# Optimization experiments

Measured on AMD Instinct MI355X. Metric: run time of the kernel, lower is better.

Reference implementation:

```python
import jax, jax.numpy as jnp
import numpy as np

N_NODES = 100000
N_EDGES = 6400000
D_IN = 512
D_HID = 16
N_CLASSES = 16


def setup_inputs() -> dict:
    key = jax.random.key(0)
    k1, k2, k3, k4, k5, k6 = jax.random.split(key, 6)
    x = jax.random.normal(k1, (N_NODES, D_IN), dtype=jnp.float32)
    edge_index = jax.random.randint(k2, (2, N_EDGES), 0, N_NODES, dtype=jnp.int64)
    # Glorot-style init for GCN weights
    W1 = jax.random.normal(k3, (D_IN, D_HID), dtype=jnp.float32) * (1.0 / np.sqrt(D_IN))
    b1 = jnp.zeros((D_HID,), dtype=jnp.float32)
    W2 = jax.random.normal(k4, (D_HID, N_CLASSES), dtype=jnp.float32) * (1.0 / np.sqrt(D_HID))
    b2 = jnp.zeros((N_CLASSES,), dtype=jnp.float32)
    return {"x": x, "W1": W1, "b1": b1, "W2": W2, "b2": b2, "edge_index": edge_index}


def reference(x, W1, b1, W2, b2, edge_index):
    N = x.shape[0]
    loops = jnp.arange(N, dtype=edge_index.dtype)
    # GCN: add self-loops, symmetric D^-1/2 A D^-1/2 normalization
    src = jnp.concatenate([edge_index[0], loops])  # [E+N]
    dst = jnp.concatenate([edge_index[1], loops])  # [E+N]
    deg = jax.ops.segment_sum(jnp.ones(src.shape[0], dtype=x.dtype), dst, num_segments=N)
    dinv = jnp.where(deg > 0, jax.lax.rsqrt(deg), 0.0)
    norm = (dinv[src] * dinv[dst])[:, None]  # [E+N, 1]

    def gcn_conv(h, W, b):
        h = h @ W                                  # [N, d_out] transform first (PyG order)
        agg = jax.ops.segment_sum(h[src] * norm, dst, num_segments=N)
        return agg + b

    h = jax.nn.relu(gcn_conv(x, W1, b1))
    # F.dropout(training=self.training) is identity in eval mode
    logits = gcn_conv(h, W2, b2)
    return jax.nn.log_softmax(logits, axis=1)
```

## Files before the change

kernel.cpp:

```cpp
#include <hip/hip_runtime.h>
#include <hip/hip_bf16.h>
#include <math.h>

#define N_NODES 100000
#define N_EDGES 6400000
#define D_IN 512
#define D_HID 16

__global__ void deg_kernel(const int* __restrict__ dst, int* __restrict__ deg) {
    int e = blockIdx.x * blockDim.x + threadIdx.x;
    if (e < N_EDGES) atomicAdd(&deg[dst[e]], 1);
}

__global__ void dinv_kernel(const int* __restrict__ deg, float* __restrict__ dinv) {
    int i = blockIdx.x * blockDim.x + threadIdx.x;
    if (i < N_NODES) dinv[i] = rsqrtf((float)deg[i] + 1.0f);
}

__global__ void scan1(const int* __restrict__ deg, int* __restrict__ row_start,
                      int* __restrict__ bsum) {
    __shared__ int sd[256];
    int tid = threadIdx.x;
    int base = blockIdx.x * 1024 + tid * 4;
    int d0 = 0, d1 = 0, d2 = 0, d3 = 0;
    if (base + 3 < N_NODES) {
        d0 = deg[base]; d1 = deg[base + 1]; d2 = deg[base + 2]; d3 = deg[base + 3];
    } else {
        if (base < N_NODES) d0 = deg[base];
        if (base + 1 < N_NODES) d1 = deg[base + 1];
        if (base + 2 < N_NODES) d2 = deg[base + 2];
    }
    int s = d0 + d1 + d2 + d3;
    sd[tid] = s;
    __syncthreads();
    for (int off = 1; off < 256; off <<= 1) {
        int v = (tid >= off) ? sd[tid - off] : 0;
        __syncthreads();
        sd[tid] += v;
        __syncthreads();
    }
    int excl = sd[tid] - s;
    if (base < N_NODES) row_start[base] = excl;
    if (base + 1 < N_NODES) row_start[base + 1] = excl + d0;
    if (base + 2 < N_NODES) row_start[base + 2] = excl + d0 + d1;
    if (base + 3 < N_NODES) row_start[base + 3] = excl + d0 + d1 + d2;
    if (tid == 255) bsum[blockIdx.x] = sd[255];
}

__global__ void scan2(int* __restrict__ bsum, int nb) {
    __shared__ int sd[128];
    int tid = threadIdx.x;
    int v = (tid < nb) ? bsum[tid] : 0;
    sd[tid] = v;
    __syncthreads();
    for (int off = 1; off < 128; off <<= 1) {
        int u = (tid >= off) ? sd[tid - off] : 0;
        __syncthreads();
        sd[tid] += u;
        __syncthreads();
    }
    if (tid < nb) bsum[tid] = sd[tid] - v;
}

__global__ void scan3(int* __restrict__ row_start, int* __restrict__ cursor,
                      const int* __restrict__ bsum) {
    int off = bsum[blockIdx.x];
    int base = blockIdx.x * 1024 + threadIdx.x * 4;
#pragma unroll
    for (int j = 0; j < 4; j++) {
        int i = base + j;
        if (i < N_NODES) {
            int v = row_start[i] + off;
            row_start[i] = v;
            cursor[i] = v;
        }
    }
}

__global__ void fill_csr(const int* __restrict__ src, const int* __restrict__ dst,
                         int* __restrict__ cursor, int* __restrict__ csr) {
    int e = blockIdx.x * blockDim.x + threadIdx.x;
    if (e < N_EDGES) {
        int d = dst[e];
        int pos = atomicAdd(&cursor[d], 1);
        csr[pos] = src[e];
    }
}

__global__ __launch_bounds__(256) void gemm1(const float* __restrict__ x,
                                             const float* __restrict__ W1,
                                             float* __restrict__ h1) {
    __shared__ float xs[256 * 33];
    int tid = threadIdx.x;
    int row0 = blockIdx.x * 256;
    int row = row0 + tid;
    float acc[16];
#pragma unroll
    for (int c = 0; c < 16; c++) acc[c] = 0.f;

    for (int k0 = 0; k0 < D_IN; k0 += 32) {
        __syncthreads();
#pragma unroll
        for (int l = 0; l < 8; l++) {
            int idx = tid + l * 256;
            int r = idx >> 3;
            int f4 = idx & 7;
            int gr = row0 + r;
            float4 v = make_float4(0.f, 0.f, 0.f, 0.f);
            if (gr < N_NODES)
                v = *(const float4*)(x + (size_t)gr * D_IN + k0 + f4 * 4);
            int a = r * 33 + f4 * 4;
            xs[a] = v.x; xs[a + 1] = v.y; xs[a + 2] = v.z; xs[a + 3] = v.w;
        }
        __syncthreads();
#pragma unroll
        for (int kk = 0; kk < 32; kk++) {
            float xv = xs[tid * 33 + kk];
            const float* wr = W1 + (k0 + kk) * 16;
#pragma unroll
            for (int c = 0; c < 16; c++) acc[c] = fmaf(xv, wr[c], acc[c]);
        }
    }
    if (row < N_NODES) {
        float4* o = (float4*)(h1 + (size_t)row * 16);
        o[0] = make_float4(acc[0], acc[1], acc[2], acc[3]);
        o[1] = make_float4(acc[4], acc[5], acc[6], acc[7]);
        o[2] = make_float4(acc[8], acc[9], acc[10], acc[11]);
        o[3] = make_float4(acc[12], acc[13], acc[14], acc[15]);
    }
}

__global__ __launch_bounds__(256) void agg1(const float* __restrict__ h1,
                                            const float* __restrict__ dinv,
                                            const int* __restrict__ row_start,
                                            const int* __restrict__ deg,
                                            const int* __restrict__ csr,
                                            const float* __restrict__ b1,
                                            const float* __restrict__ W2,
                                            float* __restrict__ h3) {
    int tid = threadIdx.x;
    int node = blockIdx.x * 16 + (tid >> 4);
    int c = tid & 15;
    if (node >= N_NODES) return;
    float di = dinv[node];
    float acc = h1[(size_t)node * 16 + c] * di * di;
    int start = row_start[node];
    int cnt = deg[node];
    int sN = 0; float vN = 0.f, dN = 0.f;
    if (cnt > 0) {
        sN = csr[start];
        vN = h1[(size_t)sN * 16 + c];
        dN = dinv[sN];
    }
    for (int t = 0; t < cnt; t++) {
        float vC = vN, dC = dN;
        if (t + 1 < cnt) {
            int s = csr[start + t + 1];
            vN = h1[(size_t)s * 16 + c];
            dN = dinv[s];
        }
        acc = fmaf(vC, dC * di, acc);
    }
    float v = acc + b1[c];
    v = v > 0.f ? v : 0.f;
    float out = 0.f;
#pragma unroll
    for (int j = 0; j < 16; j++) {
        float vj = __shfl(v, j, 16);
        out = fmaf(vj, W2[j * 16 + c], out);
    }
    h3[(size_t)node * 16 + c] = out;
}

__global__ __launch_bounds__(256) void agg2(const float* __restrict__ h3,
                                            const float* __restrict__ dinv,
                                            const int* __restrict__ row_start,
                                            const int* __restrict__ deg,
                                            const int* __restrict__ csr,
                                            const float* __restrict__ b2,
                                            float* __restrict__ out) {
    int tid = threadIdx.x;
    int node = blockIdx.x * 16 + (tid >> 4);
    int c = tid & 15;
    if (node >= N_NODES) return;
    float di = dinv[node];
    float acc = h3[(size_t)node * 16 + c] * di * di;
    int start = row_start[node];
    int cnt = deg[node];
    int sN = 0; float vN = 0.f, dN = 0.f;
    if (cnt > 0) {
        sN = csr[start];
        vN = h3[(size_t)sN * 16 + c];
        dN = dinv[sN];
    }
    for (int t = 0; t < cnt; t++) {
        float vC = vN, dC = dN;
        if (t + 1 < cnt) {
            int s = csr[start + t + 1];
            vN = h3[(size_t)s * 16 + c];
            dN = dinv[s];
        }
        acc = fmaf(vC, dC * di, acc);
    }
    float logit = acc + b2[c];
    float m = logit;
#pragma unroll
    for (int mask = 1; mask < 16; mask <<= 1)
        m = fmaxf(m, __shfl_xor(m, mask, 16));
    float e = expf(logit - m);
    float ssum = e;
#pragma unroll
    for (int mask = 1; mask < 16; mask <<= 1)
        ssum += __shfl_xor(ssum, mask, 16);
    out[(size_t)node * 16 + c] = (logit - m) - logf(ssum);
}

extern "C" void kernel_launch(void* const* d_in, const int* in_sizes, int n_in,
                              void* d_out, int out_size, void* d_ws, size_t ws_size,
                              hipStream_t stream) {
    const float* x  = (const float*)d_in[0];
    const float* W1 = (const float*)d_in[1];
    const float* b1 = (const float*)d_in[2];
    const float* W2 = (const float*)d_in[3];
    const float* b2 = (const float*)d_in[4];
    const int*   ei = (const int*)d_in[5];
    const int* src = ei;
    const int* dst = ei + N_EDGES;
    float* out = (float*)d_out;

    int* deg       = (int*)d_ws;
    int* row_start = deg + 100096;
    int* cursor    = row_start + 100096;
    float* dinv    = (float*)(cursor + 100096);
    int* bsum      = (int*)(dinv + 100096);
    int* csr       = bsum + 128;
    float* h1      = (float*)(csr + N_EDGES);
    float* h3      = h1 + 1600000;

    hipMemsetAsync(deg, 0, N_NODES * sizeof(int), stream);
    deg_kernel<<<N_EDGES / 256, 256, 0, stream>>>(dst, deg);
    dinv_kernel<<<(N_NODES + 255) / 256, 256, 0, stream>>>(deg, dinv);
    scan1<<<98, 256, 0, stream>>>(deg, row_start, bsum);
    scan2<<<1, 128, 0, stream>>>(bsum, 98);
    scan3<<<98, 256, 0, stream>>>(row_start, cursor, bsum);
    fill_csr<<<N_EDGES / 256, 256, 0, stream>>>(src, dst, cursor, csr);
    gemm1<<<(N_NODES + 255) / 256, 256, 0, stream>>>(x, W1, h1);
    agg1<<<(N_NODES + 15) / 16, 256, 0, stream>>>(h1, dinv, row_start, deg, csr, b1, W2, h3);
    agg2<<<(N_NODES + 15) / 16, 256, 0, stream>>>(h3, dinv, row_start, deg, csr, b2, out);
}
```

Before: 1.519 ms.

## Build CSR via two-level bucketed counting sort with shared-memory atomics

Replaces the global per-node atomic degree count and atomic CSR fill with a two-pass bucket sort. Edges are first histogrammed into 391 buckets of 256 destination nodes using shared-memory atomics, then scattered into a packed (src<<8 | dst&255) buffer. Per-bucket blocks then compute degrees and place edges with shared-memory atomics. This aims to cut contended global random atomics and scattered writes, at the cost of an extra 25.6MB intermediate buffer plus extra passes over the edges. The packing assumes source ids fit in 24 bits.

```diff
diff --git a/kernel.cpp b/kernel.cpp
--- a/kernel.cpp
+++ b/kernel.cpp
@@ -6,10 +6,76 @@
 #define N_EDGES 6400000
 #define D_IN 512
 #define D_HID 16
-
-__global__ void deg_kernel(const int* __restrict__ dst, int* __restrict__ deg) {
-    int e = blockIdx.x * blockDim.x + threadIdx.x;
-    if (e < N_EDGES) atomicAdd(&deg[dst[e]], 1);
+#define NB 391
+
+__global__ __launch_bounds__(256) void khist(const int* __restrict__ dst,
+                                             int* __restrict__ bhist) {
+    __shared__ int h[NB];
+    int tid = threadIdx.x;
+    for (int i = tid; i < NB; i += 256) h[i] = 0;
+    __syncthreads();
+    int base = blockIdx.x * 25600;
+#pragma unroll 4
+    for (int k = 0; k < 100; k++) {
+        int e = base + k * 256 + tid;
+        atomicAdd(&h[dst[e] >> 8], 1);
+    }
+    __syncthreads();
+    for (int i = tid; i < NB; i += 256) atomicAdd(&bhist[i], h[i]);
+}
+
+__global__ void bscan(const int* __restrict__ bhist, int* __restrict__ bbase,
+                      int* __restrict__ bcur) {
+    __shared__ int sd[512];
+    int tid = threadIdx.x;
+    int v = (tid < NB) ? bhist[tid] : 0;
+    sd[tid] = v;
+    __syncthreads();
+    for (int off = 1; off < 512; off <<= 1) {
+        int u = (tid >= off) ? sd[tid - off] : 0;
+        __syncthreads();
+        sd[tid] += u;
+        __syncthreads();
+    }
+    if (tid < NB) {
+        int excl = sd[tid] - v;
+        bbase[tid] = excl;
+        bcur[tid] = excl;
+    }
+}
+
+__global__ __launch_bounds__(256) void kscatter(const int* __restrict__ src,
+                                                const int* __restrict__ dst,
+                                                int* __restrict__ bcur,
+                                                unsigned int* __restrict__ ebuf) {
+    int e = blockIdx.x * 256 + threadIdx.x;
+    int d = dst[e];
+    int s = src[e];
+    int b = d >> 8;
+    int pos = atomicAdd(&bcur[b], 1);
+    ebuf[pos] = ((unsigned int)s << 8) | (unsigned int)(d & 255);
+}
+
+__global__ __launch_bounds__(1024) void kdeg(const unsigned int* __restrict__ ebuf,
+                                             const int* __restrict__ bhist,
+                                             const int* __restrict__ bbase,
+                                             int* __restrict__ deg) {
+    __shared__ int h[256];
+    int tid = threadIdx.x;
+    int b = blockIdx.x;
+    if (tid < 256) h[tid] = 0;
+    __syncthreads();
+    int cnt = bhist[b];
+    int start = bbase[b];
+    for (int i = tid; i < cnt; i += 1024) {
+        unsigned int v = ebuf[start + i];
+        atomicAdd(&h[v & 255u], 1);
+    }
+    __syncthreads();
+    if (tid < 256) {
+        int node = b * 256 + tid;
+        if (node < N_NODES) deg[node] = h[tid];
+    }
 }
 
 __global__ void dinv_kernel(const int* __restrict__ deg, float* __restrict__ dinv) {
@@ -62,28 +128,35 @@
     if (tid < nb) bsum[tid] = sd[tid] - v;
 }
 
-__global__ void scan3(int* __restrict__ row_start, int* __restrict__ cursor,
-                      const int* __restrict__ bsum) {
+__global__ void scan3(int* __restrict__ row_start, const int* __restrict__ bsum) {
     int off = bsum[blockIdx.x];
     int base = blockIdx.x * 1024 + threadIdx.x * 4;
 #pragma unroll
     for (int j = 0; j < 4; j++) {
         int i = base + j;
-        if (i < N_NODES) {
-            int v = row_start[i] + off;
-            row_start[i] = v;
-            cursor[i] = v;
-        }
-    }
-}
-
-__global__ void fill_csr(const int* __restrict__ src, const int* __restrict__ dst,
-                         int* __restrict__ cursor, int* __restrict__ csr) {
-    int e = blockIdx.x * blockDim.x + threadIdx.x;
-    if (e < N_EDGES) {
-        int d = dst[e];
-        int pos = atomicAdd(&cursor[d], 1);
-        csr[pos] = src[e];
+        if (i < N_NODES) row_start[i] += off;
+    }
+}
+
+__global__ __launch_bounds__(1024) void kplace(const unsigned int* __restrict__ ebuf,
+                                               const int* __restrict__ bhist,
+                                               const int* __restrict__ bbase,
+                                               const int* __restrict__ row_start,
+                                               int* __restrict__ csr) {
+    __shared__ int cur[256];
+    int tid = threadIdx.x;
+    int b = blockIdx.x;
+    if (tid < 256) {
+        int node = b * 256 + tid;
+        cur[tid] = (node < N_NODES) ? row_start[node] : 0;
+    }
+    __syncthreads();
+    int cnt = bhist[b];
+    int start = bbase[b];
+    for (int i = tid; i < cnt; i += 1024) {
+        unsigned int v = ebuf[start + i];
+        int p = atomicAdd(&cur[v & 255u], 1);
+        csr[p] = (int)(v >> 8);
     }
 }
 
@@ -229,21 +302,27 @@
     float* out = (float*)d_out;
 
     int* deg       = (int*)d_ws;
-    int* row_start = deg + 100096;
-    int* cursor    = row_start + 100096;
-    float* dinv    = (float*)(cursor + 100096);
-    int* bsum      = (int*)(dinv + 100096);
-    int* csr       = bsum + 128;
+    int* row_start = deg + 100352;
+    float* dinv    = (float*)(row_start + 100352);
+    int* bsum      = (int*)(dinv + 100352);
+    int* bhist     = bsum + 128;
+    int* bbase     = bhist + 512;
+    int* bcur      = bbase + 512;
+    unsigned int* ebuf = (unsigned int*)(bcur + 512);
+    int* csr       = (int*)(ebuf + N_EDGES);
     float* h1      = (float*)(csr + N_EDGES);
     float* h3      = h1 + 1600000;
 
-    hipMemsetAsync(deg, 0, N_NODES * sizeof(int), stream);
-    deg_kernel<<<N_EDGES / 256, 256, 0, stream>>>(dst, deg);
+    hipMemsetAsync(bhist, 0, NB * sizeof(int), stream);
+    khist<<<250, 256, 0, stream>>>(dst, bhist);
+    bscan<<<1, 512, 0, stream>>>(bhist, bbase, bcur);
+    kscatter<<<N_EDGES / 256, 256, 0, stream>>>(src, dst, bcur, ebuf);
+    kdeg<<<NB, 1024, 0, stream>>>(ebuf, bhist, bbase, deg);
     dinv_kernel<<<(N_NODES + 255) / 256, 256, 0, stream>>>(deg, dinv);
     scan1<<<98, 256, 0, stream>>>(deg, row_start, bsum);
     scan2<<<1, 128, 0, stream>>>(bsum, 98);
-    scan3<<<98, 256, 0, stream>>>(row_start, cursor, bsum);
-    fill_csr<<<N_EDGES / 256, 256, 0, stream>>>(src, dst, cursor, csr);
+    scan3<<<98, 256, 0, stream>>>(row_start, bsum);
+    kplace<<<NB, 1024, 0, stream>>>(ebuf, bhist, bbase, row_start, csr);
     gemm1<<<(N_NODES + 255) / 256, 256, 0, stream>>>(x, W1, h1);
     agg1<<<(N_NODES + 15) / 16, 256, 0, stream>>>(h1, dinv, row_start, deg, csr, b1, W2, h3);
     agg2<<<(N_NODES + 15) / 16, 256, 0, stream>>>(h3, dinv, row_start, deg, csr, b2, out);
```

Result: slower. 3.046 ms (+100.5%).

## Replace per-node CSR build with bucketed edge partition and shared-memory atomic aggregation

Applied to the files above, without the earlier changes.

Edges are no longer sorted into a per-node CSR with global atomics. Instead, a block-local histogram and two-level scan scatter them into 128-node destination buckets, packing the source index and local destination into one word. Each aggregation block then accumulates its bucket's edges with LDS atomics, and rows are prescaled by dinv in the GEMM so the per-edge dinv gather is removed. This is meant to cut global atomic contention and the scattered CSR writes, at the cost of LDS atomic contention, a larger histogram workspace, and non-deterministic summation order.

```diff
diff --git a/kernel.cpp b/kernel.cpp
--- a/kernel.cpp
+++ b/kernel.cpp
@@ -7,89 +7,129 @@
 #define D_IN 512
 #define D_HID 16
 
-__global__ void deg_kernel(const int* __restrict__ dst, int* __restrict__ deg) {
-    int e = blockIdx.x * blockDim.x + threadIdx.x;
-    if (e < N_EDGES) atomicAdd(&deg[dst[e]], 1);
-}
-
-__global__ void dinv_kernel(const int* __restrict__ deg, float* __restrict__ dinv) {
-    int i = blockIdx.x * blockDim.x + threadIdx.x;
-    if (i < N_NODES) dinv[i] = rsqrtf((float)deg[i] + 1.0f);
-}
-
-__global__ void scan1(const int* __restrict__ deg, int* __restrict__ row_start,
-                      int* __restrict__ bsum) {
+#define NBKT 782
+#define NBP  784
+#define NBLK 1000
+#define EPB  6400
+
+__global__ __launch_bounds__(256) void khist(const int* __restrict__ dst,
+                                             int* __restrict__ hist_mat) {
+    __shared__ int h[NBP];
+    int tid = threadIdx.x;
+    int blk = blockIdx.x;
+    for (int i = tid; i < NBP; i += 256) h[i] = 0;
+    __syncthreads();
+    int base = blk * EPB;
+#pragma unroll
+    for (int k = 0; k < 25; k++)
+        atomicAdd(&h[dst[base + k * 256 + tid] >> 7], 1);
+    __syncthreads();
+    for (int i = tid; i < NBKT; i += 256) hist_mat[blk * NBP + i] = h[i];
+}
+
+__global__ __launch_bounds__(256) void kbtot(const int* __restrict__ hist_mat,
+                                             int* __restrict__ btot) {
     __shared__ int sd[256];
+    int b = blockIdx.x;
+    int t = threadIdx.x;
+    int s = 0;
+    for (int r = t; r < NBLK; r += 256) s += hist_mat[r * NBP + b];
+    sd[t] = s;
+    __syncthreads();
+    for (int off = 128; off > 0; off >>= 1) {
+        if (t < off) sd[t] += sd[t + off];
+        __syncthreads();
+    }
+    if (t == 0) btot[b] = sd[0];
+}
+
+__global__ __launch_bounds__(1024) void kbscan(const int* __restrict__ btot,
+                                               int* __restrict__ bbase) {
+    __shared__ int sd[1024];
+    int t = threadIdx.x;
+    int v = (t < NBKT) ? btot[t] : 0;
+    sd[t] = v;
+    __syncthreads();
+    for (int off = 1; off < 1024; off <<= 1) {
+        int u = (t >= off) ? sd[t - off] : 0;
+        __syncthreads();
+        sd[t] += u;
+        __syncthreads();
+    }
+    if (t < NBKT) bbase[t] = sd[t] - v;
+}
+
+__global__ __launch_bounds__(256) void kbase(const int* __restrict__ hist_mat,
+                                             const int* __restrict__ bbase,
+                                             int* __restrict__ base_mat) {
+    __shared__ int sd[256];
+    __shared__ int chunk_tot;
+    int b = blockIdx.x;
+    int t = threadIdx.x;
+    int running = bbase[b];
+    for (int c0 = 0; c0 < NBLK; c0 += 256) {
+        int r = c0 + t;
+        int v = (r < NBLK) ? hist_mat[r * NBP + b] : 0;
+        sd[t] = v;
+        __syncthreads();
+        for (int off = 1; off < 256; off <<= 1) {
+            int u = (t >= off) ? sd[t - off] : 0;
+            __syncthreads();
+            sd[t] += u;
+            __syncthreads();
+        }
+        if (r < NBLK) base_mat[r * NBP + b] = running + sd[t] - v;
+        if (t == 255) chunk_tot = sd[255];
+        __syncthreads();
+        running += chunk_tot;
+        __syncthreads();
+    }
+}
+
+__global__ __launch_bounds__(256) void kscatter(const int* __restrict__ src,
+                                                const int* __restrict__ dst,
+                                                const int* __restrict__ base_mat,
+                                                unsigned int* __restrict__ ebuf) {
+    __shared__ int cur[NBP];
     int tid = threadIdx.x;
-    int base = blockIdx.x * 1024 + tid * 4;
-    int d0 = 0, d1 = 0, d2 = 0, d3 = 0;
-    if (base + 3 < N_NODES) {
-        d0 = deg[base]; d1 = deg[base + 1]; d2 = deg[base + 2]; d3 = deg[base + 3];
-    } else {
-        if (base < N_NODES) d0 = deg[base];
-        if (base + 1 < N_NODES) d1 = deg[base + 1];
-        if (base + 2 < N_NODES) d2 = deg[base + 2];
-    }
-    int s = d0 + d1 + d2 + d3;
-    sd[tid] = s;
-    __syncthreads();
-    for (int off = 1; off < 256; off <<= 1) {
-        int v = (tid >= off) ? sd[tid - off] : 0;
-        __syncthreads();
-        sd[tid] += v;
-        __syncthreads();
-    }
-    int excl = sd[tid] - s;
-    if (base < N_NODES) row_start[base] = excl;
-    if (base + 1 < N_NODES) row_start[base + 1] = excl + d0;
-    if (base + 2 < N_NODES) row_start[base + 2] = excl + d0 + d1;
-    if (base + 3 < N_NODES) row_start[base + 3] = excl + d0 + d1 + d2;
-    if (tid == 255) bsum[blockIdx.x] = sd[255];
-}
-
-__global__ void scan2(int* __restrict__ bsum, int nb) {
-    __shared__ int sd[128];
-    int tid = threadIdx.x;
-    int v = (tid < nb) ? bsum[tid] : 0;
-    sd[tid] = v;
-    __syncthreads();
-    for (int off = 1; off < 128; off <<= 1) {
-        int u = (tid >= off) ? sd[tid - off] : 0;
-        __syncthreads();
-        sd[tid] += u;
-        __syncthreads();
-    }
-    if (tid < nb) bsum[tid] = sd[tid] - v;
-}
-
-__global__ void scan3(int* __restrict__ row_start, int* __restrict__ cursor,
-                      const int* __restrict__ bsum) {
-    int off = bsum[blockIdx.x];
-    int base = blockIdx.x * 1024 + threadIdx.x * 4;
-#pragma unroll
-    for (int j = 0; j < 4; j++) {
-        int i = base + j;
-        if (i < N_NODES) {
-            int v = row_start[i] + off;
-            row_start[i] = v;
-            cursor[i] = v;
-        }
-    }
-}
-
-__global__ void fill_csr(const int* __restrict__ src, const int* __restrict__ dst,
-                         int* __restrict__ cursor, int* __restrict__ csr) {
-    int e = blockIdx.x * blockDim.x + threadIdx.x;
-    if (e < N_EDGES) {
+    int blk = blockIdx.x;
+    for (int i = tid; i < NBKT; i += 256) cur[i] = base_mat[blk * NBP + i];
+    __syncthreads();
+    int base = blk * EPB;
+#pragma unroll 4
+    for (int k = 0; k < 25; k++) {
+        int e = base + k * 256 + tid;
         int d = dst[e];
-        int pos = atomicAdd(&cursor[d], 1);
-        csr[pos] = src[e];
+        int s = src[e];
+        int p = atomicAdd(&cur[d >> 7], 1);
+        ebuf[p] = ((unsigned int)s << 7) | (unsigned int)(d & 127);
+    }
+}
+
+__global__ __launch_bounds__(256) void kdeg(const unsigned int* __restrict__ ebuf,
+                                            const int* __restrict__ btot,
+                                            const int* __restrict__ bbase,
+                                            float* __restrict__ dinv) {
+    __shared__ int h[128];
+    int t = threadIdx.x;
+    int b = blockIdx.x;
+    if (t < 128) h[t] = 0;
+    __syncthreads();
+    int cnt = btot[b];
+    int start = bbase[b];
+    for (int i = t; i < cnt; i += 256)
+        atomicAdd(&h[ebuf[start + i] & 127u], 1);
+    __syncthreads();
+    if (t < 128) {
+        int node = b * 128 + t;
+        if (node < N_NODES) dinv[node] = rsqrtf((float)h[t] + 1.0f);
     }
 }
 
 __global__ __launch_bounds__(256) void gemm1(const float* __restrict__ x,
                                              const float* __restrict__ W1,
-                                             float* __restrict__ h1) {
+                                             const float* __restrict__ dinv,
+                                             float* __restrict__ h1p) {
     __shared__ float xs[256 * 33];
     int tid = threadIdx.x;
     int row0 = blockIdx.x * 256;
@@ -122,97 +162,118 @@
         }
     }
     if (row < N_NODES) {
-        float4* o = (float4*)(h1 + (size_t)row * 16);
-        o[0] = make_float4(acc[0], acc[1], acc[2], acc[3]);
-        o[1] = make_float4(acc[4], acc[5], acc[6], acc[7]);
-        o[2] = make_float4(acc[8], acc[9], acc[10], acc[11]);
-        o[3] = make_float4(acc[12], acc[13], acc[14], acc[15]);
-    }
-}
-
-__global__ __launch_bounds__(256) void agg1(const float* __restrict__ h1,
-                                            const float* __restrict__ dinv,
-                                            const int* __restrict__ row_start,
-                                            const int* __restrict__ deg,
-                                            const int* __restrict__ csr,
-                                            const float* __restrict__ b1,
-                                            const float* __restrict__ W2,
-                                            float* __restrict__ h3) {
-    int tid = threadIdx.x;
-    int node = blockIdx.x * 16 + (tid >> 4);
-    int c = tid & 15;
-    if (node >= N_NODES) return;
-    float di = dinv[node];
-    float acc = h1[(size_t)node * 16 + c] * di * di;
-    int start = row_start[node];
-    int cnt = deg[node];
-    int sN = 0; float vN = 0.f, dN = 0.f;
-    if (cnt > 0) {
-        sN = csr[start];
-        vN = h1[(size_t)sN * 16 + c];
-        dN = dinv[sN];
-    }
-    for (int t = 0; t < cnt; t++) {
-        float vC = vN, dC = dN;
-        if (t + 1 < cnt) {
-            int s = csr[start + t + 1];
-            vN = h1[(size_t)s * 16 + c];
-            dN = dinv[s];
+        float di = dinv[row];
+        float4* o = (float4*)(h1p + (size_t)row * 16);
+        o[0] = make_float4(acc[0] * di, acc[1] * di, acc[2] * di, acc[3] * di);
+        o[1] = make_float4(acc[4] * di, acc[5] * di, acc[6] * di, acc[7] * di);
+        o[2] = make_float4(acc[8] * di, acc[9] * di, acc[10] * di, acc[11] * di);
+        o[3] = make_float4(acc[12] * di, acc[13] * di, acc[14] * di, acc[15] * di);
+    }
+}
+
+__global__ __launch_bounds__(512) void kagg1(const float* __restrict__ h1p,
+                                             const float* __restrict__ dinv,
+                                             const unsigned int* __restrict__ ebuf,
+                                             const int* __restrict__ btot,
+                                             const int* __restrict__ bbase,
+                                             const float* __restrict__ b1,
+                                             const float* __restrict__ W2,
+                                             float* __restrict__ h3p) {
+    __shared__ float acc[128 * 16];
+    __shared__ float dinvb[128];
+    __shared__ float w2s[256];
+    __shared__ float b1s[16];
+    int t = threadIdx.x;
+    int b = blockIdx.x;
+    int nb0 = b * 128;
+    if (t < 128) {
+        int n = nb0 + t;
+        dinvb[t] = (n < N_NODES) ? dinv[n] : 0.f;
+    }
+    if (t >= 128 && t < 384) w2s[t - 128] = W2[t - 128];
+    if (t >= 384 && t < 400) b1s[t - 384] = b1[t - 384];
+    for (int idx = t; idx < 2048; idx += 512) {
+        int n = nb0 + (idx >> 4);
+        acc[idx] = (n < N_NODES) ? h1p[(size_t)n * 16 + (idx & 15)] : 0.f;
+    }
+    __syncthreads();
+    int cnt = btot[b];
+    int start = bbase[b];
+    int c = t & 15;
+    for (int i = (t >> 4); i < cnt; i += 32) {
+        unsigned int e = ebuf[start + i];
+        float v = h1p[(size_t)(e >> 7) * 16 + c];
+        unsafeAtomicAdd(&acc[(e & 127u) * 16 + c], v);
+    }
+    __syncthreads();
+    for (int idx = t; idx < 2048; idx += 512) {
+        int node = idx >> 4;
+        int cc = idx & 15;
+        int gn = nb0 + node;
+        if (gn >= N_NODES) continue;
+        float di = dinvb[node];
+        float out = 0.f;
+#pragma unroll
+        for (int j = 0; j < 16; j++) {
+            float u = fmaf(di, acc[node * 16 + j], b1s[j]);
+            u = u > 0.f ? u : 0.f;
+            out = fmaf(u, w2s[j * 16 + cc], out);
         }
-        acc = fmaf(vC, dC * di, acc);
-    }
-    float v = acc + b1[c];
-    v = v > 0.f ? v : 0.f;
-    float out = 0.f;
-#pragma unroll
-    for (int j = 0; j < 16; j++) {
-        float vj = __shfl(v, j, 16);
-        out = fmaf(vj, W2[j * 16 + c], out);
-    }
-    h3[(size_t)node * 16 + c] = out;
-}
-
-__global__ __launch_bounds__(256) void agg2(const float* __restrict__ h3,
-                                            const float* __restrict__ dinv,
-                                            const int* __restrict__ row_start,
-                                            const int* __restrict__ deg,
-                                            const int* __restrict__ csr,
-                                            const float* __restrict__ b2,
-                                            float* __restrict__ out) {
-    int tid = threadIdx.x;
-    int node = blockIdx.x * 16 + (tid >> 4);
-    int c = tid & 15;
-    if (node >= N_NODES) return;
-    float di = dinv[node];
-    float acc = h3[(size_t)node * 16 + c] * di * di;
-    int start = row_start[node];
-    int cnt = deg[node];
-    int sN = 0; float vN = 0.f, dN = 0.f;
-    if (cnt > 0) {
-        sN = csr[start];
-        vN = h3[(size_t)sN * 16 + c];
-        dN = dinv[sN];
-    }
-    for (int t = 0; t < cnt; t++) {
-        float vC = vN, dC = dN;
-        if (t + 1 < cnt) {
-            int s = csr[start + t + 1];
-            vN = h3[(size_t)s * 16 + c];
-            dN = dinv[s];
-        }
-        acc = fmaf(vC, dC * di, acc);
-    }
-    float logit = acc + b2[c];
-    float m = logit;
-#pragma unroll
-    for (int mask = 1; mask < 16; mask <<= 1)
-        m = fmaxf(m, __shfl_xor(m, mask, 16));
-    float e = expf(logit - m);
-    float ssum = e;
-#pragma unroll
-    for (int mask = 1; mask < 16; mask <<= 1)
-        ssum += __shfl_xor(ssum, mask, 16);
-    out[(size_t)node * 16 + c] = (logit - m) - logf(ssum);
+        h3p[(size_t)gn * 16 + cc] = out * di;
+    }
+}
+
+__global__ __launch_bounds__(512) void kagg2(const float* __restrict__ h3p,
+                                             const float* __restrict__ dinv,
+                                             const unsigned int* __restrict__ ebuf,
+                                             const int* __restrict__ btot,
+                                             const int* __restrict__ bbase,
+                                             const float* __restrict__ b2,
+                                             float* __restrict__ out) {
+    __shared__ float acc[128 * 16];
+    __shared__ float dinvb[128];
+    __shared__ float b2s[16];
+    int t = threadIdx.x;
+    int b = blockIdx.x;
+    int nb0 = b * 128;
+    if (t < 128) {
+        int n = nb0 + t;
+        dinvb[t] = (n < N_NODES) ? dinv[n] : 0.f;
+    }
+    if (t >= 128 && t < 144) b2s[t - 128] = b2[t - 128];
+    for (int idx = t; idx < 2048; idx += 512) {
+        int n = nb0 + (idx >> 4);
+        acc[idx] = (n < N_NODES) ? h3p[(size_t)n * 16 + (idx & 15)] : 0.f;
+    }
+    __syncthreads();
+    int cnt = btot[b];
+    int start = bbase[b];
+    int c = t & 15;
+    for (int i = (t >> 4); i < cnt; i += 32) {
+        unsigned int e = ebuf[start + i];
+        float v = h3p[(size_t)(e >> 7) * 16 + c];
+        unsafeAtomicAdd(&acc[(e & 127u) * 16 + c], v);
+    }
+    __syncthreads();
+    int grp = t >> 4;
+#pragma unroll
+    for (int rep = 0; rep < 4; rep++) {
+        int node = grp + rep * 32;
+        int gn = nb0 + node;
+        float di = dinvb[node];
+        float logit = fmaf(di, acc[node * 16 + c], b2s[c]);
+        float m = logit;
+#pragma unroll
+        for (int mask = 1; mask < 16; mask <<= 1)
+            m = fmaxf(m, __shfl_xor(m, mask, 16));
+        float e = expf(logit - m);
+        float ssum = e;
+#pragma unroll
+        for (int mask = 1; mask < 16; mask <<= 1)
+            ssum += __shfl_xor(ssum, mask, 16);
+        if (gn < N_NODES)
+            out[(size_t)gn * 16 + c] = (logit - m) - logf(ssum);
+    }
 }
 
 extern "C" void kernel_launch(void* const* d_in, const int* in_sizes, int n_in,
@@ -228,23 +289,22 @@
     const int* dst = ei + N_EDGES;
     float* out = (float*)d_out;
 
-    int* deg       = (int*)d_ws;
-    int* row_start = deg + 100096;
-    int* cursor    = row_start + 100096;
-    float* dinv    = (float*)(cursor + 100096);
-    int* bsum      = (int*)(dinv + 100096);
-    int* csr       = bsum + 128;
-    float* h1      = (float*)(csr + N_EDGES);
-    float* h3      = h1 + 1600000;
-
-    hipMemsetAsync(deg, 0, N_NODES * sizeof(int), stream);
-    deg_kernel<<<N_EDGES / 256, 256, 0, stream>>>(dst, deg);
-    dinv_kernel<<<(N_NODES + 255) / 256, 256, 0, stream>>>(deg, dinv);
-    scan1<<<98, 256, 0, stream>>>(deg, row_start, bsum);
-    scan2<<<1, 128, 0, stream>>>(bsum, 98);
-    scan3<<<98, 256, 0, stream>>>(row_start, cursor, bsum);
-    fill_csr<<<N_EDGES / 256, 256, 0, stream>>>(src, dst, cursor, csr);
-    gemm1<<<(N_NODES + 255) / 256, 256, 0, stream>>>(x, W1, h1);
-    agg1<<<(N_NODES + 15) / 16, 256, 0, stream>>>(h1, dinv, row_start, deg, csr, b1, W2, h3);
-    agg2<<<(N_NODES + 15) / 16, 256, 0, stream>>>(h3, dinv, row_start, deg, csr, b2, out);
-}
+    int* hist_mat  = (int*)d_ws;
+    int* base_mat  = hist_mat + NBLK * NBP;
+    int* btot      = base_mat + NBLK * NBP;
+    int* bbase     = btot + 1024;
+    float* dinv    = (float*)(bbase + 1024);
+    unsigned int* ebuf = (unsigned int*)(dinv + 100352);
+    float* h1p     = (float*)(ebuf + N_EDGES);
+    float* h3p     = h1p + 1600000;
+
+    khist<<<NBLK, 256, 0, stream>>>(dst, hist_mat);
+    kbtot<<<NBKT, 256, 0, stream>>>(hist_mat, btot);
+    kbscan<<<1, 1024, 0, stream>>>(btot, bbase);
+    kbase<<<NBKT, 256, 0, stream>>>(hist_mat, bbase, base_mat);
+    kscatter<<<NBLK, 256, 0, stream>>>(src, dst, base_mat, ebuf);
+    kdeg<<<NBKT, 256, 0, stream>>>(ebuf, btot, bbase, dinv);
+    gemm1<<<(N_NODES + 255) / 256, 256, 0, stream>>>(x, W1, dinv, h1p);
+    kagg1<<<NBKT, 512, 0, stream>>>(h1p, dinv, ebuf, btot, bbase, b1, W2, h3p);
+    kagg2<<<NBKT, 512, 0, stream>>>(h3p, dinv, ebuf, btot, bbase, b2, out);
+}
```

After: 1.898 ms. 24.9% more time.
